# Kernel optimization log

Hardware: AMD Instinct MI355X
Metric: run time of the kernel (lower is better)

Reference implementation:

```python
import jax, jax.numpy as jnp
import numpy as np

BETA = 0.25
EPS = 1e-12

def normalise(x):
    # L2 normalise over last axis
    return x / jnp.sqrt(jnp.sum(x * x, axis=-1, keepdims=True) + EPS)

def setup_inputs() -> dict:
    key = jax.random.key(0)
    k = jax.random.split(key, 6)
    N, d, c, P = 8192, 768, 256, 16384
    return {
        "z": jax.random.normal(k[0], (N, d), dtype=jnp.float32),
        "W_in": jax.random.normal(k[1], (d, c), dtype=jnp.float32) * 0.02,
        "b_in": jnp.zeros((c,), dtype=jnp.float32),
        "W_out": jax.random.normal(k[2], (c, d), dtype=jnp.float32) * 0.02,
        "b_out": jnp.zeros((d,), dtype=jnp.float32),
        "codebook": jax.random.normal(k[3], (P, c), dtype=jnp.float32),
    }

def reference(z, W_in, b_in, W_out, b_out, codebook):
    sg = jax.lax.stop_gradient
    # input projection + L2 normalise
    zq = normalise(z @ W_in + b_in)                 # [N, c]
    cb = normalise(codebook)                        # [P, c]
    # squared euclidean distances: ||z||^2 - 2 z.c + ||c||^2
    dist = (jnp.sum(zq * zq, axis=-1, keepdims=True)
            - 2.0 * jnp.einsum('nc,pc->np', zq, cb)
            + jnp.sum(cb * cb, axis=-1)[None, :])   # [N, P]
    idxes = jnp.argmin(dist, axis=-1)               # [N]
    codes = normalise(codebook[idxes])              # gather + normalise, [N, c]
    loss = BETA * (zq - sg(codes)) ** 2 + (sg(zq) - codes) ** 2
    # straight-through estimator
    codes = zq + sg(codes - zq)
    out = codes @ W_out + b_out                     # [N, d]
    return out, loss, idxes
```

## Files before the change

kernel.cpp:

```cpp
#include <hip/hip_runtime.h>
#include <hip/hip_fp16.h>
#include <math.h>

#define NN 8192
#define DD 768
#define CC 256
#define PP 16384
#define NG 256
#define MARGIN 5.0e-3f
#define BETA_C 1.25f
#define EPS_C 1e-12f

typedef __attribute__((ext_vector_type(8))) _Float16 f16x8;
typedef __attribute__((ext_vector_type(8))) short bf16x8;
typedef __attribute__((ext_vector_type(4))) float f32x4;
typedef __attribute__((ext_vector_type(16))) float f32x16;

static __device__ __forceinline__ ushort f2h(float x) {
    _Float16 h = (_Float16)x;
    return __builtin_bit_cast(unsigned short, h);
}
static __device__ __forceinline__ ushort f2bf(float x) {
    unsigned u = __float_as_uint(x);
    return (ushort)((u + 0x7fffu + ((u >> 16) & 1u)) >> 16);
}
static __device__ __forceinline__ float bf2f(ushort h) {
    return __uint_as_float(((unsigned)h) << 16);
}

static __device__ __forceinline__ void gload_lds16(const void* g, void* l) {
    __builtin_amdgcn_global_load_lds(
        (const __attribute__((address_space(1))) unsigned int*)g,
        (__attribute__((address_space(3))) unsigned int*)l, 16, 0, 0);
}

__global__ __launch_bounds__(256) void k_gemm_in(const float* __restrict__ z,
    const float* __restrict__ W, const float* __restrict__ b,
    float* __restrict__ zq)
{
    __shared__ float zt[64][36];
    __shared__ float wt[32][68];
    const int t = threadIdx.x;
    const int ti = t >> 4, tj = t & 15;
    const int n0 = blockIdx.x * 64;
    const int c0 = blockIdx.y * 64;

    f32x4 acc[4];
#pragma unroll
    for (int r = 0; r < 4; ++r) acc[r] = (f32x4){0.f, 0.f, 0.f, 0.f};

    for (int k0 = 0; k0 < DD; k0 += 32) {
        __syncthreads();
#pragma unroll
        for (int l = 0; l < 2; ++l) {
            int idx = l * 256 + t;
            int row = idx >> 3, c4 = idx & 7;
            *reinterpret_cast<float4*>(&zt[row][c4 * 4]) =
                *reinterpret_cast<const float4*>(&z[(size_t)(n0 + row) * DD + k0 + c4 * 4]);
            int krow = idx >> 4, w4 = idx & 15;
            *reinterpret_cast<float4*>(&wt[krow][w4 * 4]) =
                *reinterpret_cast<const float4*>(&W[(size_t)(k0 + krow) * CC + c0 + w4 * 4]);
        }
        __syncthreads();
#pragma unroll
        for (int kk = 0; kk < 32; kk += 4) {
            float4 a4[4], b4[4];
#pragma unroll
            for (int r = 0; r < 4; ++r)
                a4[r] = *reinterpret_cast<const float4*>(&zt[ti * 4 + r][kk]);
#pragma unroll
            for (int q = 0; q < 4; ++q)
                b4[q] = *reinterpret_cast<const float4*>(&wt[kk + q][tj * 4]);
#pragma unroll
            for (int q = 0; q < 4; ++q)
#pragma unroll
                for (int r = 0; r < 4; ++r) {
                    float av = ((const float*)&a4[r])[q];
                    acc[r].x += av * b4[q].x;
                    acc[r].y += av * b4[q].y;
                    acc[r].z += av * b4[q].z;
                    acc[r].w += av * b4[q].w;
                }
        }
    }
#pragma unroll
    for (int r = 0; r < 4; ++r) {
        int col = c0 + tj * 4;
        float4 o;
        o.x = acc[r].x + b[col];
        o.y = acc[r].y + b[col + 1];
        o.z = acc[r].z + b[col + 2];
        o.w = acc[r].w + b[col + 3];
        *reinterpret_cast<float4*>(&zq[(size_t)(n0 + ti * 4 + r) * CC + col]) = o;
    }
}

__global__ __launch_bounds__(256) void k_norm2(const float* __restrict__ src,
    float* __restrict__ dstf32, ushort* __restrict__ dsth,
    float* __restrict__ sq, float* __restrict__ rinvout, int rows)
{
    const int wave = threadIdx.x >> 6;
    const int lane = threadIdx.x & 63;
    const int row = blockIdx.x * 4 + wave;
    if (row >= rows) return;
    float4 v = *reinterpret_cast<const float4*>(&src[(size_t)row * CC + lane * 4]);
    float s = v.x * v.x + v.y * v.y + v.z * v.z + v.w * v.w;
#pragma unroll
    for (int off = 32; off; off >>= 1) s += __shfl_xor(s, off, 64);
    float r = 1.0f / sqrtf(s + EPS_C);
    v.x *= r; v.y *= r; v.z *= r; v.w *= r;
    if (dstf32)
        *reinterpret_cast<float4*>(&dstf32[(size_t)row * CC + lane * 4]) = v;
    ushort4 hv;
    hv.x = f2h(v.x); hv.y = f2h(v.y); hv.z = f2h(v.z); hv.w = f2h(v.w);
    *reinterpret_cast<ushort4*>(&dsth[(size_t)row * CC + lane * 4]) = hv;
    if (sq) {
        float s2 = v.x * v.x + v.y * v.y + v.z * v.z + v.w * v.w;
#pragma unroll
        for (int off = 32; off; off >>= 1) s2 += __shfl_xor(s2, off, 64);
        if (lane == 0) {
            sq[row] = s2;
            if (rinvout) rinvout[row] = r;
        }
    }
}

__global__ __launch_bounds__(256) void k_split_w(const float* __restrict__ W,
    ushort* __restrict__ wthi, ushort* __restrict__ wtlo)
{
    __shared__ float tile[64][68];
    const int t = threadIdx.x;
    const int d0 = blockIdx.x * 64;
    const int k0 = blockIdx.y * 64;
#pragma unroll
    for (int i = 0; i < 16; ++i) {
        int row = i * 4 + (t >> 6);
        int col = t & 63;
        tile[row][col] = W[(size_t)(k0 + row) * DD + d0 + col];
    }
    __syncthreads();
#pragma unroll
    for (int i = 0; i < 16; ++i) {
        int drow = i * 4 + (t >> 6);
        int kc = t & 63;
        float v = tile[kc][drow];
        ushort hi = f2bf(v);
        float rres = v - bf2f(hi);
        ushort lo = f2bf(rres);
        wthi[(size_t)(d0 + drow) * CC + k0 + kc] = hi;
        wtlo[(size_t)(d0 + drow) * CC + k0 + kc] = lo;
    }
}

__global__ __launch_bounds__(256) void k_dist(
    const ushort* __restrict__ cbh, const ushort* __restrict__ zqh,
    const float* __restrict__ cz2,
    float* __restrict__ gmin, unsigned long long* __restrict__ maskA)
{
    __shared__ ushort lds[2][12288];
    const int t = threadIdx.x;
    const int lane = t & 63;
    const int w = t >> 6;
    const int wr = w >> 1;
    const int wc = w & 1;
    const int p0 = blockIdx.x * 256;
    const int n0 = blockIdx.y * 128;
    const int kh = lane >> 5;
    const int r31 = lane & 31;

    f32x16 acc[4][2];
#pragma unroll
    for (int mi = 0; mi < 4; ++mi) {
        const int pbm = p0 + wr * 128 + mi * 32;
#pragma unroll
        for (int q = 0; q < 4; ++q) {
            float4 cz = *reinterpret_cast<const float4*>(&cz2[pbm + q * 8 + kh * 4]);
#pragma unroll
            for (int j = 0; j < 4; ++j) {
                float v = -0.5f * ((const float*)&cz.x)[j];
                acc[mi][0][q * 4 + j] = v;
                acc[mi][1][q * 4 + j] = v;
            }
        }
    }

    const int u_l = lane >> 3;
    const int e = (lane & 7) ^ u_l;
    const int hh = e >> 2, jj = e & 3;
    const ushort* srcA[4];
    const ushort* srcB[2];
#pragma unroll
    for (int i = 0; i < 4; ++i)
        srcA[i] = cbh + (size_t)(p0 + 2 * (w * 32 + i * 8 + u_l) + hh) * CC + jj * 8;
#pragma unroll
    for (int i = 0; i < 2; ++i)
        srcB[i] = zqh + (size_t)(n0 + 2 * (w * 16 + i * 8 + u_l) + hh) * CC + jj * 8;

#define STAGE(buf, kt)                                                        \
    {                                                                         \
        _Pragma("unroll")                                                     \
        for (int i = 0; i < 4; ++i)                                           \
            gload_lds16(srcA[i] + (kt) * 32, &lds[buf][(w * 32 + i * 8) * 64]); \
        _Pragma("unroll")                                                     \
        for (int i = 0; i < 2; ++i)                                           \
            gload_lds16(srcB[i] + (kt) * 32, &lds[buf][8192 + (w * 16 + i * 8) * 64]); \
    }

    const int ua = wr * 64 + (r31 >> 1);
    const int ub = wc * 32 + (r31 >> 1);
    const int hb = (r31 & 1) * 4 + kh;

    STAGE(0, 0);
    __syncthreads();

    for (int kt = 0; kt < 8; ++kt) {
        const int cur = kt & 1;
        if (kt < 7) STAGE(cur ^ 1, kt + 1);
#pragma unroll
        for (int ks = 0; ks < 2; ++ks) {
            f16x8 af[4], bfv[2];
#pragma unroll
            for (int mi = 0; mi < 4; ++mi) {
                int u = ua + mi * 16;
                af[mi] = *reinterpret_cast<const f16x8*>(
                    &lds[cur][u * 64 + (((hb + ks * 2) ^ (u & 7)) * 8)]);
            }
#pragma unroll
            for (int ni = 0; ni < 2; ++ni) {
                int u = ub + ni * 16;
                bfv[ni] = *reinterpret_cast<const f16x8*>(
                    &lds[cur][8192 + u * 64 + (((hb + ks * 2) ^ (u & 7)) * 8)]);
            }
            __builtin_amdgcn_s_setprio(1);
#pragma unroll
            for (int mi = 0; mi < 4; ++mi)
#pragma unroll
                for (int ni = 0; ni < 2; ++ni)
                    acc[mi][ni] = __builtin_amdgcn_mfma_f32_32x32x16_f16(
                        af[mi], bfv[ni], acc[mi][ni], 0, 0, 0);
            __builtin_amdgcn_s_setprio(0);
        }
        if (kt < 7) __syncthreads();
    }
#undef STAGE

#pragma unroll
    for (int ni = 0; ni < 2; ++ni) {
#pragma unroll
        for (int g = 0; g < 2; ++g) {
            float M = -1e30f;
#pragma unroll
            for (int m2 = 0; m2 < 2; ++m2)
#pragma unroll
                for (int r = 0; r < 16; ++r) M = fmaxf(M, acc[g * 2 + m2][ni][r]);
            M = fmaxf(M, __shfl_xor(M, 32, 64));
            const float thr = M - 0.5f * MARGIN;
            unsigned long long msk = 0ull;
#pragma unroll
            for (int m2 = 0; m2 < 2; ++m2)
#pragma unroll
                for (int q = 0; q < 4; ++q) {
                    unsigned nib = 0u;
#pragma unroll
                    for (int j = 0; j < 4; ++j)
                        nib |= (acc[g * 2 + m2][ni][q * 4 + j] >= thr) ? (1u << j) : 0u;
                    msk |= (unsigned long long)nib << (m2 * 32 + q * 8 + kh * 4);
                }
            msk |= __shfl_xor(msk, 32, 64);
            if (kh == 0) {
                int n = n0 + wc * 64 + ni * 32 + r31;
                int grp = (p0 >> 6) + wr * 2 + g;
                gmin[(size_t)n * NG + grp] = -2.0f * M;
                maskA[(size_t)n * NG + grp] = msk;
            }
        }
    }
}

__global__ __launch_bounds__(256) void k_pick(
    const float* __restrict__ gmin, const unsigned long long* __restrict__ maskA,
    const float* __restrict__ zqn, const float* __restrict__ cb_raw,
    const float* __restrict__ rinv, const float* __restrict__ cz2,
    float* __restrict__ idxf, int* __restrict__ idxi)
{
    __shared__ int lst[4][256];
    __shared__ int cnt[4];
    const int t = threadIdx.x;
    const int w = t >> 6;
    const int lane = t & 63;
    const int row = blockIdx.x * 4 + w;

    float4 zr = *reinterpret_cast<const float4*>(&zqn[(size_t)row * CC + lane * 4]);
    float4 gv = *reinterpret_cast<const float4*>(&gmin[(size_t)row * NG + lane * 4]);

    float pm = fminf(fminf(gv.x, gv.y), fminf(gv.z, gv.w));
#pragma unroll
    for (int off = 1; off < 64; off <<= 1) pm = fminf(pm, __shfl_xor(pm, off, 64));
    const float thresh = pm + MARGIN;

    if (lane == 0) cnt[w] = 0;
    __syncthreads();
    {
        const float g4[4] = {gv.x, gv.y, gv.z, gv.w};
#pragma unroll
        for (int j = 0; j < 4; ++j)
            if (g4[j] <= thresh) {
                int pos = atomicAdd(&cnt[w], 1);
                lst[w][pos] = lane * 4 + j;
            }
    }
    __syncthreads();

    const int nc = cnt[w];
    unsigned long long best = ~0ull;
    for (int ci = 0; ci < nc; ++ci) {
        int g = lst[w][ci];
        unsigned long long msk = maskA[(size_t)row * NG + g];
        while (msk) {
            int bit = __ffsll((long long)msk) - 1;
            msk &= msk - 1;
            int p = g * 64 + bit;
            float rv = rinv[p];
            float4 c4 = *reinterpret_cast<const float4*>(&cb_raw[(size_t)p * CC + lane * 4]);
            float part = (c4.x * rv) * zr.x + (c4.y * rv) * zr.y
                       + (c4.z * rv) * zr.z + (c4.w * rv) * zr.w;
#pragma unroll
            for (int off = 1; off < 64; off <<= 1) part += __shfl_xor(part, off, 64);
            float d4 = fmaf(-2.0f, part, 4.0f + cz2[p]);
            unsigned long long pk = ((unsigned long long)__float_as_uint(d4) << 32) | (unsigned)p;
            best = best < pk ? best : pk;
        }
    }
    if (lane == 0) {
        int p = (int)(best & 0xffffffffu);
        idxf[row] = (float)p;
        idxi[row] = p;
    }
}

__global__ __launch_bounds__(256) void k_codes(const float* __restrict__ zqn,
    const float* __restrict__ cb_raw, const float* __restrict__ rinv,
    const int* __restrict__ idxv, ushort* __restrict__ chi,
    ushort* __restrict__ clo, float* __restrict__ loss)
{
    int idx = blockIdx.x * 256 + threadIdx.x;
    int n = idx >> 6;
    int c4 = idx & 63;
    int p = idxv[n];
    float rv = rinv[p];
    float4 cv = *reinterpret_cast<const float4*>(&cb_raw[(size_t)p * CC + c4 * 4]);
    cv.x *= rv; cv.y *= rv; cv.z *= rv; cv.w *= rv;
    ushort4 hv, lv16;
    {
        hv.x = f2bf(cv.x); lv16.x = f2bf(cv.x - bf2f(hv.x));
        hv.y = f2bf(cv.y); lv16.y = f2bf(cv.y - bf2f(hv.y));
        hv.z = f2bf(cv.z); lv16.z = f2bf(cv.z - bf2f(hv.z));
        hv.w = f2bf(cv.w); lv16.w = f2bf(cv.w - bf2f(hv.w));
    }
    *reinterpret_cast<ushort4*>(&chi[(size_t)n * CC + c4 * 4]) = hv;
    *reinterpret_cast<ushort4*>(&clo[(size_t)n * CC + c4 * 4]) = lv16;
    float4 zv = *reinterpret_cast<const float4*>(&zqn[(size_t)n * CC + c4 * 4]);
    float4 lsv;
    float dx = zv.x - cv.x, dy = zv.y - cv.y, dz = zv.z - cv.z, dw = zv.w - cv.w;
    lsv.x = BETA_C * dx * dx; lsv.y = BETA_C * dy * dy;
    lsv.z = BETA_C * dz * dz; lsv.w = BETA_C * dw * dw;
    *reinterpret_cast<float4*>(&loss[(size_t)n * CC + c4 * 4]) = lsv;
}

__global__ __launch_bounds__(256) void k_gemm_out_mfma(
    const ushort* __restrict__ chi, const ushort* __restrict__ clo,
    const ushort* __restrict__ wthi, const ushort* __restrict__ wtlo,
    const float* __restrict__ bout, float* __restrict__ out)
{
    __shared__ ushort sAh[128 * 64];
    __shared__ ushort sAl[128 * 64];
    __shared__ ushort sBh[128 * 64];
    __shared__ ushort sBl[128 * 64];
    const int t = threadIdx.x;
    const int lane = t & 63;
    const int w = t >> 6;
    const int wr = w >> 1;
    const int wc = w & 1;
    const int nb = blockIdx.x * 128;
    const int db = blockIdx.y * 128;
    const int kh = lane >> 5;
    const int r31 = lane & 31;

    f32x16 acc[2][2];
#pragma unroll
    for (int mi = 0; mi < 2; ++mi)
#pragma unroll
        for (int ni = 0; ni < 2; ++ni)
#pragma unroll
            for (int r = 0; r < 16; ++r) acc[mi][ni][r] = 0.f;

    const int srow = lane >> 3;
    const int schunk = (lane & 7) ^ srow;
    const size_t rowA = (size_t)(nb + w * 32 + srow) * CC;
    const size_t rowB = (size_t)(db + w * 32 + srow) * CC;
    const char* sAhsrc = (const char*)chi + rowA * 2 + schunk * 16;
    const char* sAlsrc = (const char*)clo + rowA * 2 + schunk * 16;
    const char* sBhsrc = (const char*)wthi + rowB * 2 + schunk * 16;
    const char* sBlsrc = (const char*)wtlo + rowB * 2 + schunk * 16;
    char* dA = (char*)sAh + (w * 32) * 128;
    char* dAl = (char*)sAl + (w * 32) * 128;
    char* dB = (char*)sBh + (w * 32) * 128;
    char* dBl = (char*)sBl + (w * 32) * 128;

    const int sx = (r31 & 7) << 4;

    for (int k0 = 0; k0 < CC; k0 += 64) {
        __syncthreads();
#pragma unroll
        for (int i = 0; i < 4; ++i) {
            gload_lds16(sAhsrc + (size_t)i * 8 * (CC * 2) + k0 * 2, dA + i * 1024);
            gload_lds16(sAlsrc + (size_t)i * 8 * (CC * 2) + k0 * 2, dAl + i * 1024);
            gload_lds16(sBhsrc + (size_t)i * 8 * (CC * 2) + k0 * 2, dB + i * 1024);
            gload_lds16(sBlsrc + (size_t)i * 8 * (CC * 2) + k0 * 2, dBl + i * 1024);
        }
        __syncthreads();
#pragma unroll
        for (int ks = 0; ks < 4; ++ks) {
            const int ko = ((ks * 32 + kh * 16) ^ sx);
            bf16x8 ah[2], al[2], bh[2], bl[2];
#pragma unroll
            for (int mi = 0; mi < 2; ++mi) {
                ah[mi] = *reinterpret_cast<const bf16x8*>(
                    (const char*)sAh + (wr * 64 + mi * 32 + r31) * 128 + ko);
                al[mi] = *reinterpret_cast<const bf16x8*>(
                    (const char*)sAl + (wr * 64 + mi * 32 + r31) * 128 + ko);
            }
#pragma unroll
            for (int ni = 0; ni < 2; ++ni) {
                bh[ni] = *reinterpret_cast<const bf16x8*>(
                    (const char*)sBh + (wc * 64 + ni * 32 + r31) * 128 + ko);
                bl[ni] = *reinterpret_cast<const bf16x8*>(
                    (const char*)sBl + (wc * 64 + ni * 32 + r31) * 128 + ko);
            }
#pragma unroll
            for (int mi = 0; mi < 2; ++mi)
#pragma unroll
                for (int ni = 0; ni < 2; ++ni) {
                    acc[mi][ni] = __builtin_amdgcn_mfma_f32_32x32x16_bf16(
                        ah[mi], bh[ni], acc[mi][ni], 0, 0, 0);
                    acc[mi][ni] = __builtin_amdgcn_mfma_f32_32x32x16_bf16(
                        ah[mi], bl[ni], acc[mi][ni], 0, 0, 0);
                    acc[mi][ni] = __builtin_amdgcn_mfma_f32_32x32x16_bf16(
                        al[mi], bh[ni], acc[mi][ni], 0, 0, 0);
                }
        }
    }

#pragma unroll
    for (int ni = 0; ni < 2; ++ni) {
        const int d = db + wc * 64 + ni * 32 + r31;
        const float bv = bout[d];
#pragma unroll
        for (int mi = 0; mi < 2; ++mi) {
            const int nbase = nb + wr * 64 + mi * 32 + 4 * kh;
#pragma unroll
            for (int q = 0; q < 4; ++q)
#pragma unroll
                for (int j = 0; j < 4; ++j) {
                    int n = nbase + j + 8 * q;
                    out[(size_t)n * DD + d] = acc[mi][ni][q * 4 + j] + bv;
                }
        }
    }
}

extern "C" void kernel_launch(void* const* d_in, const int* in_sizes, int n_in,
                              void* d_out, int out_size, void* d_ws, size_t ws_size,
                              hipStream_t stream)
{
    const float* z        = (const float*)d_in[0];
    const float* W_in     = (const float*)d_in[1];
    const float* b_in     = (const float*)d_in[2];
    const float* W_out    = (const float*)d_in[3];
    const float* b_out    = (const float*)d_in[4];
    const float* codebook = (const float*)d_in[5];

    char* ws = (char*)d_ws;
    ushort* zqh   = (ushort*)(ws);
    ushort* cbh   = (ushort*)(ws + 4194304);
    ushort* chi   = (ushort*)(ws + 12582912);
    ushort* clo   = (ushort*)(ws + 16777216);
    ushort* wthi  = (ushort*)(ws + 20971520);
    ushort* wtlo  = (ushort*)(ws + 21364736);
    float*  cz2   = (float*)(ws + 21757952);
    float*  rinv  = (float*)(ws + 21823488);
    int*    idxi  = (int*)  (ws + 21889024);

    float* out  = (float*)d_out;
    float* loss = out + (size_t)NN * DD;
    float* idxf = loss + (size_t)NN * CC;

    float* gmin = (float*)d_out;
    unsigned long long* maskA = (unsigned long long*)((char*)d_out + 8388608);
    float* zq = loss;

    k_gemm_in<<<dim3(NN / 64, CC / 64), 256, 0, stream>>>(z, W_in, b_in, zq);
    k_norm2<<<NN / 4, 256, 0, stream>>>(zq, zq, zqh, (float*)nullptr, (float*)nullptr, NN);
    k_norm2<<<PP / 4, 256, 0, stream>>>(codebook, (float*)nullptr, cbh, cz2, rinv, PP);
    k_split_w<<<dim3(DD / 64, CC / 64), 256, 0, stream>>>(W_out, wthi, wtlo);
    k_dist<<<dim3(PP / 256, NN / 128), 256, 0, stream>>>(cbh, zqh, cz2, gmin, maskA);
    k_pick<<<NN / 4, 256, 0, stream>>>(gmin, maskA, zq, codebook, rinv, cz2, idxf, idxi);
    k_codes<<<(NN * CC / 4) / 256, 256, 0, stream>>>(zq, codebook, rinv, idxi, chi, clo, loss);
    k_gemm_out_mfma<<<dim3(NN / 128, DD / 128), 256, 0, stream>>>(chi, clo, wthi, wtlo, b_out, out);
}
```

Measured before the change: 189.0 us.

## Fuse code gather and loss into pick kernel; hand-pipeline dist K loop

Removes the separate k_codes kernel. k_pick now writes the normalised code in bf16 hi/lo form and the loss directly, using the zq row it already holds in registers. This saves one launch, the idx round-trip and a re-read of zq. The dist GEMM main loop is fully unrolled with explicit vmcnt waits and raw s_barrier plus sched_barrier so the next prefetch can stay in flight during compute. The hand-written waitcnt must match the number of outstanding loads; the pipelining change carries a correctness and scheduling risk.

```diff
diff --git a/kernel.cpp b/kernel.cpp
--- a/kernel.cpp
+++ b/kernel.cpp
@@ -196,52 +196,73 @@
     for (int i = 0; i < 2; ++i)
         srcB[i] = zqh + (size_t)(n0 + 2 * (w * 16 + i * 8 + u_l) + hh) * CC + jj * 8;
 
-#define STAGE(buf, kt)                                                        \
+#define STAGE(BUF, KT)                                                        \
     {                                                                         \
         _Pragma("unroll")                                                     \
         for (int i = 0; i < 4; ++i)                                           \
-            gload_lds16(srcA[i] + (kt) * 32, &lds[buf][(w * 32 + i * 8) * 64]); \
+            gload_lds16(srcA[i] + (KT) * 32, &lds[BUF][(w * 32 + i * 8) * 64]); \
         _Pragma("unroll")                                                     \
         for (int i = 0; i < 2; ++i)                                           \
-            gload_lds16(srcB[i] + (kt) * 32, &lds[buf][8192 + (w * 16 + i * 8) * 64]); \
+            gload_lds16(srcB[i] + (KT) * 32, &lds[BUF][8192 + (w * 16 + i * 8) * 64]); \
     }
 
     const int ua = wr * 64 + (r31 >> 1);
     const int ub = wc * 32 + (r31 >> 1);
     const int hb = (r31 & 1) * 4 + kh;
 
+#define COMPUTE(BUF)                                                          \
+    {                                                                         \
+        _Pragma("unroll")                                                     \
+        for (int ks = 0; ks < 2; ++ks) {                                      \
+            f16x8 af[4], bfv[2];                                              \
+            _Pragma("unroll")                                                 \
+            for (int mi = 0; mi < 4; ++mi) {                                  \
+                int u = ua + mi * 16;                                         \
+                af[mi] = *reinterpret_cast<const f16x8*>(                     \
+                    &lds[BUF][u * 64 + (((hb + ks * 2) ^ (u & 7)) * 8)]);     \
+            }                                                                 \
+            _Pragma("unroll")                                                 \
+            for (int ni = 0; ni < 2; ++ni) {                                  \
+                int u = ub + ni * 16;                                         \
+                bfv[ni] = *reinterpret_cast<const f16x8*>(                    \
+                    &lds[BUF][8192 + u * 64 + (((hb + ks * 2) ^ (u & 7)) * 8)]); \
+            }                                                                 \
+            __builtin_amdgcn_s_setprio(1);                                    \
+            acc[0][0] = __builtin_amdgcn_mfma_f32_32x32x16_f16(af[0], bfv[0], acc[0][0], 0, 0, 0); \
+            acc[0][1] = __builtin_amdgcn_mfma_f32_32x32x16_f16(af[0], bfv[1], acc[0][1], 0, 0, 0); \
+            acc[1][0] = __builtin_amdgcn_mfma_f32_32x32x16_f16(af[1], bfv[0], acc[1][0], 0, 0, 0); \
+            acc[1][1] = __builtin_amdgcn_mfma_f32_32x32x16_f16(af[1], bfv[1], acc[1][1], 0, 0, 0); \
+            acc[2][0] = __builtin_amdgcn_mfma_f32_32x32x16_f16(af[2], bfv[0], acc[2][0], 0, 0, 0); \
+            acc[2][1] = __builtin_amdgcn_mfma_f32_32x32x16_f16(af[2], bfv[1], acc[2][1], 0, 0, 0); \
+            acc[3][0] = __builtin_amdgcn_mfma_f32_32x32x16_f16(af[3], bfv[0], acc[3][0], 0, 0, 0); \
+            acc[3][1] = __builtin_amdgcn_mfma_f32_32x32x16_f16(af[3], bfv[1], acc[3][1], 0, 0, 0); \
+            __builtin_amdgcn_s_setprio(0);                                    \
+        }                                                                     \
+    }
+
+#define BODY(KT, VM, DOSTAGE)                                                 \
+    {                                                                         \
+        if (DOSTAGE) STAGE(((KT) + 1) & 1, (KT) + 1);                         \
+        __builtin_amdgcn_sched_barrier(0);                                    \
+        asm volatile("s_waitcnt vmcnt(" #VM ")" ::: "memory");                \
+        __builtin_amdgcn_s_barrier();                                         \
+        __builtin_amdgcn_sched_barrier(0);                                    \
+        COMPUTE((KT) & 1);                                                    \
+        if ((KT) < 7) __builtin_amdgcn_s_barrier();                           \
+    }
+
     STAGE(0, 0);
-    __syncthreads();
-
-    for (int kt = 0; kt < 8; ++kt) {
-        const int cur = kt & 1;
-        if (kt < 7) STAGE(cur ^ 1, kt + 1);
-#pragma unroll
-        for (int ks = 0; ks < 2; ++ks) {
-            f16x8 af[4], bfv[2];
-#pragma unroll
-            for (int mi = 0; mi < 4; ++mi) {
-                int u = ua + mi * 16;
-                af[mi] = *reinterpret_cast<const f16x8*>(
-                    &lds[cur][u * 64 + (((hb + ks * 2) ^ (u & 7)) * 8)]);
-            }
-#pragma unroll
-            for (int ni = 0; ni < 2; ++ni) {
-                int u = ub + ni * 16;
-                bfv[ni] = *reinterpret_cast<const f16x8*>(
-                    &lds[cur][8192 + u * 64 + (((hb + ks * 2) ^ (u & 7)) * 8)]);
-            }
-            __builtin_amdgcn_s_setprio(1);
-#pragma unroll
-            for (int mi = 0; mi < 4; ++mi)
-#pragma unroll
-                for (int ni = 0; ni < 2; ++ni)
-                    acc[mi][ni] = __builtin_amdgcn_mfma_f32_32x32x16_f16(
-                        af[mi], bfv[ni], acc[mi][ni], 0, 0, 0);
-            __builtin_amdgcn_s_setprio(0);
-        }
-        if (kt < 7) __syncthreads();
-    }
+    BODY(0, 6, 1)
+    BODY(1, 6, 1)
+    BODY(2, 6, 1)
+    BODY(3, 6, 1)
+    BODY(4, 6, 1)
+    BODY(5, 6, 1)
+    BODY(6, 6, 1)
+    BODY(7, 0, 0)
+
+#undef BODY
+#undef COMPUTE
 #undef STAGE
 
 #pragma unroll
@@ -281,7 +302,8 @@
     const float* __restrict__ gmin, const unsigned long long* __restrict__ maskA,
     const float* __restrict__ zqn, const float* __restrict__ cb_raw,
     const float* __restrict__ rinv, const float* __restrict__ cz2,
-    float* __restrict__ idxf, int* __restrict__ idxi)
+    float* __restrict__ idxf, ushort* __restrict__ chi,
+    ushort* __restrict__ clo, float* __restrict__ loss)
 {
     __shared__ int lst[4][256];
     __shared__ int cnt[4];
@@ -331,40 +353,24 @@
             best = best < pk ? best : pk;
         }
     }
-    if (lane == 0) {
-        int p = (int)(best & 0xffffffffu);
-        idxf[row] = (float)p;
-        idxi[row] = p;
-    }
-}
-
-__global__ __launch_bounds__(256) void k_codes(const float* __restrict__ zqn,
-    const float* __restrict__ cb_raw, const float* __restrict__ rinv,
-    const int* __restrict__ idxv, ushort* __restrict__ chi,
-    ushort* __restrict__ clo, float* __restrict__ loss)
-{
-    int idx = blockIdx.x * 256 + threadIdx.x;
-    int n = idx >> 6;
-    int c4 = idx & 63;
-    int p = idxv[n];
-    float rv = rinv[p];
-    float4 cv = *reinterpret_cast<const float4*>(&cb_raw[(size_t)p * CC + c4 * 4]);
+    const int p = (int)(best & 0xffffffffu);
+    if (lane == 0) idxf[row] = (float)p;
+
+    const float rv = rinv[p];
+    float4 cv = *reinterpret_cast<const float4*>(&cb_raw[(size_t)p * CC + lane * 4]);
     cv.x *= rv; cv.y *= rv; cv.z *= rv; cv.w *= rv;
     ushort4 hv, lv16;
-    {
-        hv.x = f2bf(cv.x); lv16.x = f2bf(cv.x - bf2f(hv.x));
-        hv.y = f2bf(cv.y); lv16.y = f2bf(cv.y - bf2f(hv.y));
-        hv.z = f2bf(cv.z); lv16.z = f2bf(cv.z - bf2f(hv.z));
-        hv.w = f2bf(cv.w); lv16.w = f2bf(cv.w - bf2f(hv.w));
-    }
-    *reinterpret_cast<ushort4*>(&chi[(size_t)n * CC + c4 * 4]) = hv;
-    *reinterpret_cast<ushort4*>(&clo[(size_t)n * CC + c4 * 4]) = lv16;
-    float4 zv = *reinterpret_cast<const float4*>(&zqn[(size_t)n * CC + c4 * 4]);
+    hv.x = f2bf(cv.x); lv16.x = f2bf(cv.x - bf2f(hv.x));
+    hv.y = f2bf(cv.y); lv16.y = f2bf(cv.y - bf2f(hv.y));
+    hv.z = f2bf(cv.z); lv16.z = f2bf(cv.z - bf2f(hv.z));
+    hv.w = f2bf(cv.w); lv16.w = f2bf(cv.w - bf2f(hv.w));
+    *reinterpret_cast<ushort4*>(&chi[(size_t)row * CC + lane * 4]) = hv;
+    *reinterpret_cast<ushort4*>(&clo[(size_t)row * CC + lane * 4]) = lv16;
     float4 lsv;
-    float dx = zv.x - cv.x, dy = zv.y - cv.y, dz = zv.z - cv.z, dw = zv.w - cv.w;
+    float dx = zr.x - cv.x, dy = zr.y - cv.y, dz = zr.z - cv.z, dw = zr.w - cv.w;
     lsv.x = BETA_C * dx * dx; lsv.y = BETA_C * dy * dy;
     lsv.z = BETA_C * dz * dz; lsv.w = BETA_C * dw * dw;
-    *reinterpret_cast<float4*>(&loss[(size_t)n * CC + c4 * 4]) = lsv;
+    *reinterpret_cast<float4*>(&loss[(size_t)row * CC + lane * 4]) = lsv;
 }
 
 __global__ __launch_bounds__(256) void k_gemm_out_mfma(
@@ -489,7 +495,6 @@
     ushort* wtlo  = (ushort*)(ws + 21364736);
     float*  cz2   = (float*)(ws + 21757952);
     float*  rinv  = (float*)(ws + 21823488);
-    int*    idxi  = (int*)  (ws + 21889024);
 
     float* out  = (float*)d_out;
     float* loss = out + (size_t)NN * DD;
@@ -504,7 +509,7 @@
     k_norm2<<<PP / 4, 256, 0, stream>>>(codebook, (float*)nullptr, cbh, cz2, rinv, PP);
     k_split_w<<<dim3(DD / 64, CC / 64), 256, 0, stream>>>(W_out, wthi, wtlo);
     k_dist<<<dim3(PP / 256, NN / 128), 256, 0, stream>>>(cbh, zqh, cz2, gmin, maskA);
-    k_pick<<<NN / 4, 256, 0, stream>>>(gmin, maskA, zq, codebook, rinv, cz2, idxf, idxi);
-    k_codes<<<(NN * CC / 4) / 256, 256, 0, stream>>>(zq, codebook, rinv, idxi, chi, clo, loss);
+    k_pick<<<NN / 4, 256, 0, stream>>>(gmin, maskA, zq, codebook, rinv, cz2,
+                                       idxf, chi, clo, loss);
     k_gemm_out_mfma<<<dim3(NN / 128, DD / 128), 256, 0, stream>>>(chi, clo, wthi, wtlo, b_out, out);
 }
```

Result: no change. 187.1 us (-1.0%).
